# Kernel optimization log

Measured on AMD Instinct MI355X. Metric: run time of the kernel, lower is better.

The kernel has to match this reference:

```python
import jax, jax.numpy as jnp
import numpy as np

N = 100000          # num_nodes
E = 1600000         # num_edges
D_IN = 128          # in_channels
H = 128             # hidden_channels
D_OUT = 128         # out_channels


def setup_inputs() -> dict:
    key = jax.random.key(0)
    ks = jax.random.split(key, 12)
    s = 1.0 / np.sqrt(H)
    inp = {
        "x": jax.random.normal(ks[0], (N, D_IN), dtype=jnp.float32),
        "edge_index": jax.random.randint(ks[1], (2, E), 0, N, dtype=jnp.int64),
        "edge_weight": jax.random.uniform(ks[2], (E,), dtype=jnp.float32),
        # edge_lin (SparseLinear): weight [num_nodes, hidden], bias [hidden]
        "W_edge": jax.random.uniform(ks[3], (N, H), jnp.float32, -1.0 / np.sqrt(N), 1.0 / np.sqrt(N)),
        "b_edge": jax.random.uniform(ks[4], (H,), jnp.float32, -1.0 / np.sqrt(N), 1.0 / np.sqrt(N)),
        # node_mlp: single Linear(in_channels, hidden)
        "W_node": jax.random.uniform(ks[5], (D_IN, H), jnp.float32, -1.0 / np.sqrt(D_IN), 1.0 / np.sqrt(D_IN)),
        "b_node": jax.random.uniform(ks[6], (H,), jnp.float32, -1.0 / np.sqrt(D_IN), 1.0 / np.sqrt(D_IN)),
        # cat_lin1 / cat_lin2: Linear(hidden, hidden)
        "W_cat1": jax.random.uniform(ks[7], (H, H), jnp.float32, -s, s),
        "b_cat1": jax.random.uniform(ks[8], (H,), jnp.float32, -s, s),
        "W_cat2": jax.random.uniform(ks[9], (H, H), jnp.float32, -s, s),
        "b_cat2": jax.random.uniform(ks[10], (H,), jnp.float32, -s, s),
        # final_mlp: single Linear(hidden, out_channels)
        "W_final": jax.random.uniform(ks[11], (H, D_OUT), jnp.float32, -s, s),
        "b_final": jax.random.uniform(jax.random.fold_in(key, 99), (D_OUT,), jnp.float32, -s, s),
    }
    return inp


def reference(x, edge_index, edge_weight, W_edge, b_edge, W_node, b_node,
              W_cat1, b_cat1, W_cat2, b_cat2, W_final, b_final):
    num_nodes = W_edge.shape[0]
    src, dst = edge_index[0], edge_index[1]
    # SparseLinear: out[i] = sum_{(j,i)} edge_weight * W_edge[j]  (SpMM A @ W)
    msg = edge_weight[:, None] * W_edge[src]                      # [E, H]
    out = jax.ops.segment_sum(msg, dst, num_segments=num_nodes)  # [N, H]
    out = out + b_edge
    # out = out + cat_lin1(out)
    out = out + out @ W_cat1 + b_cat1
    # x branch: node_mlp (single linear), then residual adds
    xh = x @ W_node + b_node                                      # [N, H]
    out = out + xh
    out = out + xh @ W_cat2 + b_cat2
    # final_mlp(relu(out)): single linear
    return jax.nn.relu(out) @ W_final + b_final
```

## Files before the change

### kernel.cpp

```cpp
#include <hip/hip_runtime.h>
#include <hip/hip_fp16.h>

#define NN 100000
#define NE 1600000
#define H  128
#define CAP 48

typedef short short8 __attribute__((ext_vector_type(8)));
typedef float f32x4 __attribute__((ext_vector_type(4)));

__device__ __forceinline__ unsigned short f2bf(float f) {
    unsigned int u = __float_as_uint(f);
    u = (u + 0x7fffu + ((u >> 16) & 1u)) >> 16;
    return (unsigned short)u;
}
__device__ __forceinline__ unsigned int packbf(float a, float b) {
    return (unsigned int)f2bf(a) | ((unsigned int)f2bf(b) << 16);
}
__device__ __forceinline__ unsigned char f2e5m2(float f) {
    unsigned short h = __half_as_ushort(__float2half_rn(f));
    h = (unsigned short)(h + 0x7F + ((h >> 8) & 1));
    return (unsigned char)(h >> 8);
}
__device__ __forceinline__ float e5m2lo(unsigned int u) {
    return __half2float(__ushort_as_half((unsigned short)((u << 8) & 0xFF00)));
}
__device__ __forceinline__ float e5m2hi(unsigned int u) {
    return __half2float(__ushort_as_half((unsigned short)(u & 0xFF00)));
}
__device__ __forceinline__ float entw(unsigned int e) {
    return __half2float(__ushort_as_half((unsigned short)((e & 0x7FFFu) << 1)));
}

__global__ void fill_kernel(const int* __restrict__ ei, const float* __restrict__ ew,
                            int* __restrict__ deg, unsigned int* __restrict__ bkt) {
    int e = blockIdx.x * 256 + threadIdx.x;
    if (e >= NE) return;
    int d = ei[NE + e];
    int pos = atomicAdd(&deg[d], 1);
    if (pos < CAP) {
        unsigned short h = __half_as_ushort(__float2half_rn(ew[e]));
        bkt[d * CAP + pos] = ((unsigned int)ei[e] << 15) | (h >> 1);
    }
}

__global__ __launch_bounds__(128) void prep_weights(const float* __restrict__ W_node,
                                                    const float* __restrict__ W_cat1,
                                                    const float* __restrict__ W_cat2,
                                                    const float* __restrict__ W_final,
                                                    const float* __restrict__ b_edge,
                                                    const float* __restrict__ b_node,
                                                    const float* __restrict__ b_cat1,
                                                    const float* __restrict__ b_cat2,
                                                    unsigned short* __restrict__ m2_t,
                                                    unsigned short* __restrict__ w3_t,
                                                    unsigned short* __restrict__ wf_t,
                                                    float* __restrict__ b4,
                                                    int* __restrict__ deg) {
    int t = threadIdx.x;
    int n = blockIdx.x;
    if (n < H) {
        __shared__ float c2col[H];
        c2col[t] = W_cat2[t * H + n];
        __syncthreads();
        float dot = 0.f;
        #pragma unroll 8
        for (int j = 0; j < H; ++j)
            dot += W_node[t * H + j] * c2col[j];
        float w3 = W_node[t * H + n] + dot;
        m2_t[n * H + t] = f2bf(W_cat1[t * H + n] + (t == n ? 1.f : 0.f));
        w3_t[n * H + t] = f2bf(w3);
        wf_t[n * H + t] = f2bf(W_final[t * H + n]);
    } else if (n == H) {
        __shared__ float be[H], bn[H];
        be[t] = b_edge[t];
        bn[t] = b_node[t];
        __syncthreads();
        float acc = be[t] + bn[t] + b_cat1[t] + b_cat2[t];
        for (int j = 0; j < H; ++j)
            acc += be[j] * W_cat1[j * H + t] + bn[j] * W_cat2[j * H + t];
        b4[t] = acc;
    } else {
        int i = (n - H - 1) * 128 + t;
        if (i < NN) deg[i] = 0;
    }
}

__global__ __launch_bounds__(256) void gemm_we2(const float* __restrict__ W_edge,
                                                const unsigned short* __restrict__ m2_t,
                                                unsigned char* __restrict__ we8,
                                                int nrows) {
    const int TR = 32;
    __shared__ unsigned int Wsb[TR][64];
    int row0 = blockIdx.x * TR;
    int tid = threadIdx.x;

    for (int i = tid; i < TR * H / 4; i += 256) {
        int fi = i * 4;
        int rr = fi >> 7, cc = fi & 127;
        float4 v = {0.f, 0.f, 0.f, 0.f};
        if (row0 + rr < nrows)
            v = *reinterpret_cast<const float4*>(&W_edge[(long long)(row0 + rr) * H + cc]);
        int sw = (rr & 7) << 2;
        Wsb[rr][(cc >> 1) ^ sw]       = packbf(v.x, v.y);
        Wsb[rr][((cc >> 1) + 1) ^ sw] = packbf(v.z, v.w);
    }
    __syncthreads();

    int wv = tid >> 6, lane = tid & 63;
    int rt = wv & 1, ctb = (tid >> 7) * 4;
    int l15 = lane & 15, lhi = lane >> 4;
    int arow = rt * 16 + l15, asw = arow & 7;

    f32x4 zero4 = {0.f, 0.f, 0.f, 0.f};
    f32x4 acc[4];
    acc[0] = zero4; acc[1] = zero4; acc[2] = zero4; acc[3] = zero4;
    const short8* wrow = reinterpret_cast<const short8*>(&Wsb[arow][0]);

    #pragma unroll
    for (int kt = 0; kt < 4; ++kt) {
        short8 afrag = wrow[(kt * 4 + lhi) ^ asw];
        #pragma unroll
        for (int j = 0; j < 4; ++j) {
            short8 bfrag = *reinterpret_cast<const short8*>(
                &m2_t[((ctb + j) * 16 + l15) * H + kt * 32 + lhi * 8]);
            acc[j] = __builtin_amdgcn_mfma_f32_16x16x32_bf16(afrag, bfrag, acc[j], 0, 0, 0);
        }
    }

    #pragma unroll
    for (int j = 0; j < 4; ++j) {
        int colg = (ctb + j) * 16 + l15;
        #pragma unroll
        for (int r = 0; r < 4; ++r) {
            int row = row0 + rt * 16 + lhi * 4 + r;
            if (row < nrows)
                we8[(long long)row * H + colg] = f2e5m2(acc[j][r]);
        }
    }
}

#define EDGE2(jv, ax, ay)                                                   \
    {                                                                       \
        unsigned int e0 = bkt[jv];                                          \
        unsigned int e1 = bkt[jv + 1];                                      \
        unsigned int u0 = we8u[(e0 >> 15) * 64 + lane];                     \
        unsigned int u1 = we8u[(e1 >> 15) * 64 + lane];                     \
        float w0 = entw(e0), w1 = entw(e1);                                 \
        ax += w0 * e5m2lo(u0) + w1 * e5m2lo(u1);                            \
        ay += w0 * e5m2hi(u0) + w1 * e5m2hi(u1);                            \
    }

#define EDGE1(jv, ax, ay)                                                   \
    {                                                                       \
        unsigned int e = bkt[jv];                                           \
        unsigned int u = we8u[(e >> 15) * 64 + lane];                       \
        float w = entw(e);                                                  \
        ax += w * e5m2lo(u);                                                \
        ay += w * e5m2hi(u);                                                \
    }

#define STEP8(eN0, eN1, uN0, uN1, jv, ax, ay)                               \
    {                                                                       \
        float w0 = entw(eN0), w1 = entw(eN1);                               \
        ax += w0 * e5m2lo(uN0) + w1 * e5m2lo(uN1);                          \
        ay += w0 * e5m2hi(uN0) + w1 * e5m2hi(uN1);                          \
        jv += 2;                                                            \
    }

__global__ __launch_bounds__(256) void gather_fused(const int* __restrict__ deg,
                                                    const unsigned int* __restrict__ bkt,
                                                    const unsigned short* __restrict__ we8u,
                                                    const float* __restrict__ x,
                                                    const unsigned short* __restrict__ w3_t,
                                                    const float* __restrict__ b4,
                                                    const unsigned short* __restrict__ wf_t,
                                                    const float* __restrict__ bf,
                                                    float* __restrict__ out,
                                                    int nrows) {
    const int TR = 32;
    __shared__ unsigned int Xsb[TR][64];
    __shared__ float Gs[TR][132];
    int row0 = blockIdx.x * TR;
    int tid = threadIdx.x;

    for (int i = tid; i < TR * H / 4; i += 256) {
        int fi = i * 4;
        int rr = fi >> 7, cc = fi & 127;
        float4 xv = *reinterpret_cast<const float4*>(&x[(long long)(row0 + rr) * H + cc]);
        int sw = (rr & 7) << 2;
        Xsb[rr][(cc >> 1) ^ sw]       = packbf(xv.x, xv.y);
        Xsb[rr][((cc >> 1) + 1) ^ sw] = packbf(xv.z, xv.w);
    }

    int wv = tid >> 6;
    int lane = tid & 63;
    {
        int base = row0 + wv * 8;
        float axA = 0.f, ayA = 0.f, axB = 0.f, ayB = 0.f;
        float axC = 0.f, ayC = 0.f, axD = 0.f, ayD = 0.f;
        float axE = 0.f, ayE = 0.f, axF = 0.f, ayF = 0.f;
        float axG = 0.f, ayG = 0.f, axH = 0.f, ayH = 0.f;

        int dgA = __builtin_amdgcn_readfirstlane(deg[base]);
        int dgB = __builtin_amdgcn_readfirstlane(deg[base + 1]);
        int dgC = __builtin_amdgcn_readfirstlane(deg[base + 2]);
        int dgD = __builtin_amdgcn_readfirstlane(deg[base + 3]);
        int dgE = __builtin_amdgcn_readfirstlane(deg[base + 4]);
        int dgF = __builtin_amdgcn_readfirstlane(deg[base + 5]);
        int dgG = __builtin_amdgcn_readfirstlane(deg[base + 6]);
        int dgH = __builtin_amdgcn_readfirstlane(deg[base + 7]);
        if (dgA > CAP) dgA = CAP;
        if (dgB > CAP) dgB = CAP;
        if (dgC > CAP) dgC = CAP;
        if (dgD > CAP) dgD = CAP;
        if (dgE > CAP) dgE = CAP;
        if (dgF > CAP) dgF = CAP;
        if (dgG > CAP) dgG = CAP;
        if (dgH > CAP) dgH = CAP;
        int jA = base * CAP,        i1A = jA + dgA;
        int jB = (base + 1) * CAP,  i1B = jB + dgB;
        int jC = (base + 2) * CAP,  i1C = jC + dgC;
        int jD = (base + 3) * CAP,  i1D = jD + dgD;
        int jE = (base + 4) * CAP,  i1E = jE + dgE;
        int jF = (base + 5) * CAP,  i1F = jF + dgF;
        int jG = (base + 6) * CAP,  i1G = jG + dgG;
        int jH = (base + 7) * CAP,  i1H = jH + dgH;

        while (jA + 2 <= i1A && jB + 2 <= i1B && jC + 2 <= i1C && jD + 2 <= i1D &&
               jE + 2 <= i1E && jF + 2 <= i1F && jG + 2 <= i1G && jH + 2 <= i1H) {
            unsigned int eA0 = bkt[jA], eA1 = bkt[jA + 1];
            unsigned int eB0 = bkt[jB], eB1 = bkt[jB + 1];
            unsigned int eC0 = bkt[jC], eC1 = bkt[jC + 1];
            unsigned int eD0 = bkt[jD], eD1 = bkt[jD + 1];
            unsigned int eE0 = bkt[jE], eE1 = bkt[jE + 1];
            unsigned int eF0 = bkt[jF], eF1 = bkt[jF + 1];
            unsigned int eG0 = bkt[jG], eG1 = bkt[jG + 1];
            unsigned int eH0 = bkt[jH], eH1 = bkt[jH + 1];
            unsigned int uA0 = we8u[(eA0 >> 15) * 64 + lane];
            unsigned int uA1 = we8u[(eA1 >> 15) * 64 + lane];
            unsigned int uB0 = we8u[(eB0 >> 15) * 64 + lane];
            unsigned int uB1 = we8u[(eB1 >> 15) * 64 + lane];
            unsigned int uC0 = we8u[(eC0 >> 15) * 64 + lane];
            unsigned int uC1 = we8u[(eC1 >> 15) * 64 + lane];
            unsigned int uD0 = we8u[(eD0 >> 15) * 64 + lane];
            unsigned int uD1 = we8u[(eD1 >> 15) * 64 + lane];
            unsigned int uE0 = we8u[(eE0 >> 15) * 64 + lane];
            unsigned int uE1 = we8u[(eE1 >> 15) * 64 + lane];
            unsigned int uF0 = we8u[(eF0 >> 15) * 64 + lane];
            unsigned int uF1 = we8u[(eF1 >> 15) * 64 + lane];
            unsigned int uG0 = we8u[(eG0 >> 15) * 64 + lane];
            unsigned int uG1 = we8u[(eG1 >> 15) * 64 + lane];
            unsigned int uH0 = we8u[(eH0 >> 15) * 64 + lane];
            unsigned int uH1 = we8u[(eH1 >> 15) * 64 + lane];
            STEP8(eA0, eA1, uA0, uA1, jA, axA, ayA)
            STEP8(eB0, eB1, uB0, uB1, jB, axB, ayB)
            STEP8(eC0, eC1, uC0, uC1, jC, axC, ayC)
            STEP8(eD0, eD1, uD0, uD1, jD, axD, ayD)
            STEP8(eE0, eE1, uE0, uE1, jE, axE, ayE)
            STEP8(eF0, eF1, uF0, uF1, jF, axF, ayF)
            STEP8(eG0, eG1, uG0, uG1, jG, axG, ayG)
            STEP8(eH0, eH1, uH0, uH1, jH, axH, ayH)
        }
        while (jA + 2 <= i1A && jB + 2 <= i1B) { EDGE2(jA, axA, ayA) EDGE2(jB, axB, ayB) jA += 2; jB += 2; }
        for (; jA + 2 <= i1A; jA += 2) EDGE2(jA, axA, ayA)
        if (jA < i1A) EDGE1(jA, axA, ayA)
        for (; jB + 2 <= i1B; jB += 2) EDGE2(jB, axB, ayB)
        if (jB < i1B) EDGE1(jB, axB, ayB)
        while (jC + 2 <= i1C && jD + 2 <= i1D) { EDGE2(jC, axC, ayC) EDGE2(jD, axD, ayD) jC += 2; jD += 2; }
        for (; jC + 2 <= i1C; jC += 2) EDGE2(jC, axC, ayC)
        if (jC < i1C) EDGE1(jC, axC, ayC)
        for (; jD + 2 <= i1D; jD += 2) EDGE2(jD, axD, ayD)
        if (jD < i1D) EDGE1(jD, axD, ayD)
        while (jE + 2 <= i1E && jF + 2 <= i1F) { EDGE2(jE, axE, ayE) EDGE2(jF, axF, ayF) jE += 2; jF += 2; }
        for (; jE + 2 <= i1E; jE += 2) EDGE2(jE, axE, ayE)
        if (jE < i1E) EDGE1(jE, axE, ayE)
        for (; jF + 2 <= i1F; jF += 2) EDGE2(jF, axF, ayF)
        if (jF < i1F) EDGE1(jF, axF, ayF)
        while (jG + 2 <= i1G && jH + 2 <= i1H) { EDGE2(jG, axG, ayG) EDGE2(jH, axH, ayH) jG += 2; jH += 2; }
        for (; jG + 2 <= i1G; jG += 2) EDGE2(jG, axG, ayG)
        if (jG < i1G) EDGE1(jG, axG, ayG)
        for (; jH + 2 <= i1H; jH += 2) EDGE2(jH, axH, ayH)
        if (jH < i1H) EDGE1(jH, axH, ayH)

        int rr = wv * 8;
        *reinterpret_cast<float2*>(&Gs[rr][2 * lane])     = make_float2(axA, ayA);
        *reinterpret_cast<float2*>(&Gs[rr + 1][2 * lane]) = make_float2(axB, ayB);
        *reinterpret_cast<float2*>(&Gs[rr + 2][2 * lane]) = make_float2(axC, ayC);
        *reinterpret_cast<float2*>(&Gs[rr + 3][2 * lane]) = make_float2(axD, ayD);
        *reinterpret_cast<float2*>(&Gs[rr + 4][2 * lane]) = make_float2(axE, ayE);
        *reinterpret_cast<float2*>(&Gs[rr + 5][2 * lane]) = make_float2(axF, ayF);
        *reinterpret_cast<float2*>(&Gs[rr + 6][2 * lane]) = make_float2(axG, ayG);
        *reinterpret_cast<float2*>(&Gs[rr + 7][2 * lane]) = make_float2(axH, ayH);
    }
    __syncthreads();

    int rt = wv & 1, ctb = (tid >> 7) * 4;
    int l15 = lane & 15, lhi = lane >> 4;
    int arow = rt * 16 + l15, asw = arow & 7;

    f32x4 acc[4];
    #pragma unroll
    for (int j = 0; j < 4; ++j) {
        int colg = (ctb + j) * 16 + l15;
        float bv = b4[colg];
        #pragma unroll
        for (int r = 0; r < 4; ++r)
            acc[j][r] = Gs[rt * 16 + lhi * 4 + r][colg] + bv;
    }
    __syncthreads();

    const short8* xsrow = reinterpret_cast<const short8*>(&Xsb[arow][0]);
    #pragma unroll
    for (int kt = 0; kt < 4; ++kt) {
        short8 afrag = xsrow[(kt * 4 + lhi) ^ asw];
        #pragma unroll
        for (int j = 0; j < 4; ++j) {
            short8 bfrag = *reinterpret_cast<const short8*>(
                &w3_t[((ctb + j) * 16 + l15) * H + kt * 32 + lhi * 8]);
            acc[j] = __builtin_amdgcn_mfma_f32_16x16x32_bf16(afrag, bfrag, acc[j], 0, 0, 0);
        }
    }

    unsigned short* t4s = reinterpret_cast<unsigned short*>(Gs);
    #pragma unroll
    for (int j = 0; j < 4; ++j) {
        int colg = (ctb + j) * 16 + l15;
        #pragma unroll
        for (int r = 0; r < 4; ++r) {
            int row = rt * 16 + lhi * 4 + r;
            float v = fmaxf(acc[j][r], 0.f);
            t4s[row * 128 + (colg ^ ((row & 7) << 3))] = f2bf(v);
        }
    }
    __syncthreads();

    f32x4 zero4 = {0.f, 0.f, 0.f, 0.f};
    f32x4 acc2[4];
    acc2[0] = zero4; acc2[1] = zero4; acc2[2] = zero4; acc2[3] = zero4;
    const short8* t4row = reinterpret_cast<const short8*>(t4s + arow * 128);

    #pragma unroll
    for (int kt = 0; kt < 4; ++kt) {
        short8 afrag = t4row[(kt * 4 + lhi) ^ asw];
        #pragma unroll
        for (int j = 0; j < 4; ++j) {
            short8 bfrag = *reinterpret_cast<const short8*>(
                &wf_t[((ctb + j) * 16 + l15) * H + kt * 32 + lhi * 8]);
            acc2[j] = __builtin_amdgcn_mfma_f32_16x16x32_bf16(afrag, bfrag, acc2[j], 0, 0, 0);
        }
    }

    #pragma unroll
    for (int j = 0; j < 4; ++j) {
        int colg = (ctb + j) * 16 + l15;
        float bv = bf[colg];
        #pragma unroll
        for (int r = 0; r < 4; ++r) {
            int row = row0 + rt * 16 + lhi * 4 + r;
            out[(long long)row * H + colg] = acc2[j][r] + bv;
        }
    }
}

extern "C" void kernel_launch(void* const* d_in, const int* in_sizes, int n_in,
                              void* d_out, int out_size, void* d_ws, size_t ws_size,
                              hipStream_t stream) {
    const float* x       = (const float*)d_in[0];
    const int*   ei      = (const int*)d_in[1];
    const float* ew      = (const float*)d_in[2];
    const float* W_edge  = (const float*)d_in[3];
    const float* b_edge  = (const float*)d_in[4];
    const float* W_node  = (const float*)d_in[5];
    const float* b_node  = (const float*)d_in[6];
    const float* W_cat1  = (const float*)d_in[7];
    const float* b_cat1  = (const float*)d_in[8];
    const float* W_cat2  = (const float*)d_in[9];
    const float* b_cat2  = (const float*)d_in[10];
    const float* W_final = (const float*)d_in[11];
    const float* b_final = (const float*)d_in[12];
    float* out = (float*)d_out;

    int* deg = (int*)d_ws;
    unsigned int* bkt = (unsigned int*)(deg + NN);
    unsigned char* we8 = (unsigned char*)(bkt + (size_t)NN * CAP);
    unsigned short* m2_t = (unsigned short*)(we8 + (size_t)NN * H);
    unsigned short* w3_t = m2_t + H * H;
    unsigned short* wf_t = w3_t + H * H;
    float* b4 = (float*)(wf_t + H * H);

    int zero_blocks = (NN + 127) / 128;
    prep_weights<<<H + 1 + zero_blocks, H, 0, stream>>>(W_node, W_cat1, W_cat2, W_final,
                                                        b_edge, b_node, b_cat1, b_cat2,
                                                        m2_t, w3_t, wf_t, b4, deg);
    fill_kernel<<<(NE + 255) / 256, 256, 0, stream>>>(ei, ew, deg, bkt);

    gemm_we2<<<(NN + 31) / 32, 256, 0, stream>>>(W_edge, m2_t, we8, NN);

    gather_fused<<<(NN + 31) / 32, 256, 0, stream>>>(deg, bkt, (const unsigned short*)we8,
                                                     x, w3_t, b4, wf_t, b_final, out, NN);
}
```

Baseline: 297.2 us.

## Move cat_lin1 GEMM after aggregation and merge W_edge conversion into prep kernel

Instead of precomputing W_edge·(I+W_cat1) over all 100k rows before the gather, W_edge is simply quantised to e5m2 in a combined prep kernel. The aggregated rows are packed to bf16 in shared memory and multiplied by m2 via MFMA inside the fused gather kernel, alongside the x·w3 product. This removes the separate GEMM kernel launch and its dependency on prepared weights. The cost is extra MFMA work and B-fragment loads per block in the gather kernel, plus bf16 rounding of the aggregated sums.

```diff
diff --git a/kernel.cpp b/kernel.cpp
--- a/kernel.cpp
+++ b/kernel.cpp
@@ -5,6 +5,9 @@
 #define NE 1600000
 #define H  128
 #define CAP 48
+#define CONV_BLKS 6250
+#define PREP_BLKS 64
+#define ZERO_BLKS ((NN + 255) / 256)
 
 typedef short short8 __attribute__((ext_vector_type(8)));
 typedef float f32x4 __attribute__((ext_vector_type(4)));
@@ -30,6 +33,71 @@
 }
 __device__ __forceinline__ float entw(unsigned int e) {
     return __half2float(__ushort_as_half((unsigned short)((e & 0x7FFFu) << 1)));
+}
+
+__global__ __launch_bounds__(256) void conv_prep(const float* __restrict__ W_edge,
+                                                 const float* __restrict__ W_node,
+                                                 const float* __restrict__ W_cat1,
+                                                 const float* __restrict__ W_cat2,
+                                                 const float* __restrict__ W_final,
+                                                 const float* __restrict__ b_edge,
+                                                 const float* __restrict__ b_node,
+                                                 const float* __restrict__ b_cat1,
+                                                 const float* __restrict__ b_cat2,
+                                                 unsigned char* __restrict__ we8,
+                                                 unsigned short* __restrict__ m2_t,
+                                                 unsigned short* __restrict__ w3_t,
+                                                 unsigned short* __restrict__ wf_t,
+                                                 float* __restrict__ b4,
+                                                 int* __restrict__ deg) {
+    int b = blockIdx.x;
+    int t = threadIdx.x;
+    if (b < CONV_BLKS) {
+        long long i = (long long)b * 2048 + t * 8;
+        float4 v0 = *reinterpret_cast<const float4*>(&W_edge[i]);
+        float4 v1 = *reinterpret_cast<const float4*>(&W_edge[i + 4]);
+        unsigned long long o = 0;
+        o |= (unsigned long long)f2e5m2(v0.x);
+        o |= (unsigned long long)f2e5m2(v0.y) << 8;
+        o |= (unsigned long long)f2e5m2(v0.z) << 16;
+        o |= (unsigned long long)f2e5m2(v0.w) << 24;
+        o |= (unsigned long long)f2e5m2(v1.x) << 32;
+        o |= (unsigned long long)f2e5m2(v1.y) << 40;
+        o |= (unsigned long long)f2e5m2(v1.z) << 48;
+        o |= (unsigned long long)f2e5m2(v1.w) << 56;
+        *reinterpret_cast<unsigned long long*>(&we8[i]) = o;
+    } else if (b < CONV_BLKS + PREP_BLKS) {
+        int p = b - CONV_BLKS;
+        int half = t >> 7, tt = t & 127;
+        int n = p * 2 + half;
+        __shared__ float c2col[2][H];
+        c2col[half][tt] = W_cat2[tt * H + n];
+        __syncthreads();
+        float dot = 0.f;
+        #pragma unroll 8
+        for (int j = 0; j < H; ++j)
+            dot += W_node[tt * H + j] * c2col[half][j];
+        float w3 = W_node[tt * H + n] + dot;
+        m2_t[n * H + tt] = f2bf(W_cat1[tt * H + n] + (tt == n ? 1.f : 0.f));
+        w3_t[n * H + tt] = f2bf(w3);
+        wf_t[n * H + tt] = f2bf(W_final[tt * H + n]);
+    } else if (b == CONV_BLKS + PREP_BLKS) {
+        __shared__ float be[H], bn[H];
+        if (t < H) {
+            be[t] = b_edge[t];
+            bn[t] = b_node[t];
+        }
+        __syncthreads();
+        if (t < H) {
+            float acc = be[t] + bn[t] + b_cat1[t] + b_cat2[t];
+            for (int j = 0; j < H; ++j)
+                acc += be[j] * W_cat1[j * H + t] + bn[j] * W_cat2[j * H + t];
+            b4[t] = acc;
+        }
+    } else {
+        int i = (b - CONV_BLKS - PREP_BLKS - 1) * 256 + t;
+        if (i < NN) deg[i] = 0;
+    }
 }
 
 __global__ void fill_kernel(const int* __restrict__ ei, const float* __restrict__ ew,
@@ -44,102 +112,6 @@
     }
 }
 
-__global__ __launch_bounds__(128) void prep_weights(const float* __restrict__ W_node,
-                                                    const float* __restrict__ W_cat1,
-                                                    const float* __restrict__ W_cat2,
-                                                    const float* __restrict__ W_final,
-                                                    const float* __restrict__ b_edge,
-                                                    const float* __restrict__ b_node,
-                                                    const float* __restrict__ b_cat1,
-                                                    const float* __restrict__ b_cat2,
-                                                    unsigned short* __restrict__ m2_t,
-                                                    unsigned short* __restrict__ w3_t,
-                                                    unsigned short* __restrict__ wf_t,
-                                                    float* __restrict__ b4,
-                                                    int* __restrict__ deg) {
-    int t = threadIdx.x;
-    int n = blockIdx.x;
-    if (n < H) {
-        __shared__ float c2col[H];
-        c2col[t] = W_cat2[t * H + n];
-        __syncthreads();
-        float dot = 0.f;
-        #pragma unroll 8
-        for (int j = 0; j < H; ++j)
-            dot += W_node[t * H + j] * c2col[j];
-        float w3 = W_node[t * H + n] + dot;
-        m2_t[n * H + t] = f2bf(W_cat1[t * H + n] + (t == n ? 1.f : 0.f));
-        w3_t[n * H + t] = f2bf(w3);
-        wf_t[n * H + t] = f2bf(W_final[t * H + n]);
-    } else if (n == H) {
-        __shared__ float be[H], bn[H];
-        be[t] = b_edge[t];
-        bn[t] = b_node[t];
-        __syncthreads();
-        float acc = be[t] + bn[t] + b_cat1[t] + b_cat2[t];
-        for (int j = 0; j < H; ++j)
-            acc += be[j] * W_cat1[j * H + t] + bn[j] * W_cat2[j * H + t];
-        b4[t] = acc;
-    } else {
-        int i = (n - H - 1) * 128 + t;
-        if (i < NN) deg[i] = 0;
-    }
-}
-
-__global__ __launch_bounds__(256) void gemm_we2(const float* __restrict__ W_edge,
-                                                const unsigned short* __restrict__ m2_t,
-                                                unsigned char* __restrict__ we8,
-                                                int nrows) {
-    const int TR = 32;
-    __shared__ unsigned int Wsb[TR][64];
-    int row0 = blockIdx.x * TR;
-    int tid = threadIdx.x;
-
-    for (int i = tid; i < TR * H / 4; i += 256) {
-        int fi = i * 4;
-        int rr = fi >> 7, cc = fi & 127;
-        float4 v = {0.f, 0.f, 0.f, 0.f};
-        if (row0 + rr < nrows)
-            v = *reinterpret_cast<const float4*>(&W_edge[(long long)(row0 + rr) * H + cc]);
-        int sw = (rr & 7) << 2;
-        Wsb[rr][(cc >> 1) ^ sw]       = packbf(v.x, v.y);
-        Wsb[rr][((cc >> 1) + 1) ^ sw] = packbf(v.z, v.w);
-    }
-    __syncthreads();
-
-    int wv = tid >> 6, lane = tid & 63;
-    int rt = wv & 1, ctb = (tid >> 7) * 4;
-    int l15 = lane & 15, lhi = lane >> 4;
-    int arow = rt * 16 + l15, asw = arow & 7;
-
-    f32x4 zero4 = {0.f, 0.f, 0.f, 0.f};
-    f32x4 acc[4];
-    acc[0] = zero4; acc[1] = zero4; acc[2] = zero4; acc[3] = zero4;
-    const short8* wrow = reinterpret_cast<const short8*>(&Wsb[arow][0]);
-
-    #pragma unroll
-    for (int kt = 0; kt < 4; ++kt) {
-        short8 afrag = wrow[(kt * 4 + lhi) ^ asw];
-        #pragma unroll
-        for (int j = 0; j < 4; ++j) {
-            short8 bfrag = *reinterpret_cast<const short8*>(
-                &m2_t[((ctb + j) * 16 + l15) * H + kt * 32 + lhi * 8]);
-            acc[j] = __builtin_amdgcn_mfma_f32_16x16x32_bf16(afrag, bfrag, acc[j], 0, 0, 0);
-        }
-    }
-
-    #pragma unroll
-    for (int j = 0; j < 4; ++j) {
-        int colg = (ctb + j) * 16 + l15;
-        #pragma unroll
-        for (int r = 0; r < 4; ++r) {
-            int row = row0 + rt * 16 + lhi * 4 + r;
-            if (row < nrows)
-                we8[(long long)row * H + colg] = f2e5m2(acc[j][r]);
-        }
-    }
-}
-
 #define EDGE2(jv, ax, ay)                                                   \
     {                                                                       \
         unsigned int e0 = bkt[jv];                                          \
@@ -172,6 +144,7 @@
                                                     const unsigned int* __restrict__ bkt,
                                                     const unsigned short* __restrict__ we8u,
                                                     const float* __restrict__ x,
+                                                    const unsigned short* __restrict__ m2_t,
                                                     const unsigned short* __restrict__ w3_t,
                                                     const float* __restrict__ b4,
                                                     const unsigned short* __restrict__ wf_t,
@@ -180,7 +153,7 @@
                                                     int nrows) {
     const int TR = 32;
     __shared__ unsigned int Xsb[TR][64];
-    __shared__ float Gs[TR][132];
+    __shared__ unsigned int Gsb[TR][64];
     int row0 = blockIdx.x * TR;
     int tid = threadIdx.x;
 
@@ -284,14 +257,14 @@
         if (jH < i1H) EDGE1(jH, axH, ayH)
 
         int rr = wv * 8;
-        *reinterpret_cast<float2*>(&Gs[rr][2 * lane])     = make_float2(axA, ayA);
-        *reinterpret_cast<float2*>(&Gs[rr + 1][2 * lane]) = make_float2(axB, ayB);
-        *reinterpret_cast<float2*>(&Gs[rr + 2][2 * lane]) = make_float2(axC, ayC);
-        *reinterpret_cast<float2*>(&Gs[rr + 3][2 * lane]) = make_float2(axD, ayD);
-        *reinterpret_cast<float2*>(&Gs[rr + 4][2 * lane]) = make_float2(axE, ayE);
-        *reinterpret_cast<float2*>(&Gs[rr + 5][2 * lane]) = make_float2(axF, ayF);
-        *reinterpret_cast<float2*>(&Gs[rr + 6][2 * lane]) = make_float2(axG, ayG);
-        *reinterpret_cast<float2*>(&Gs[rr + 7][2 * lane]) = make_float2(axH, ayH);
+        Gsb[rr][lane ^ ((rr & 7) << 2)]             = packbf(axA, ayA);
+        Gsb[rr + 1][lane ^ (((rr + 1) & 7) << 2)]   = packbf(axB, ayB);
+        Gsb[rr + 2][lane ^ (((rr + 2) & 7) << 2)]   = packbf(axC, ayC);
+        Gsb[rr + 3][lane ^ (((rr + 3) & 7) << 2)]   = packbf(axD, ayD);
+        Gsb[rr + 4][lane ^ (((rr + 4) & 7) << 2)]   = packbf(axE, ayE);
+        Gsb[rr + 5][lane ^ (((rr + 5) & 7) << 2)]   = packbf(axF, ayF);
+        Gsb[rr + 6][lane ^ (((rr + 6) & 7) << 2)]   = packbf(axG, ayG);
+        Gsb[rr + 7][lane ^ (((rr + 7) & 7) << 2)]   = packbf(axH, ayH);
     }
     __syncthreads();
 
@@ -302,27 +275,29 @@
     f32x4 acc[4];
     #pragma unroll
     for (int j = 0; j < 4; ++j) {
-        int colg = (ctb + j) * 16 + l15;
-        float bv = b4[colg];
-        #pragma unroll
-        for (int r = 0; r < 4; ++r)
-            acc[j][r] = Gs[rt * 16 + lhi * 4 + r][colg] + bv;
-    }
-    __syncthreads();
-
+        float bv = b4[(ctb + j) * 16 + l15];
+        acc[j][0] = bv; acc[j][1] = bv; acc[j][2] = bv; acc[j][3] = bv;
+    }
+
+    const short8* gsrow = reinterpret_cast<const short8*>(&Gsb[arow][0]);
     const short8* xsrow = reinterpret_cast<const short8*>(&Xsb[arow][0]);
     #pragma unroll
     for (int kt = 0; kt < 4; ++kt) {
-        short8 afrag = xsrow[(kt * 4 + lhi) ^ asw];
+        short8 afragG = gsrow[(kt * 4 + lhi) ^ asw];
+        short8 afragX = xsrow[(kt * 4 + lhi) ^ asw];
         #pragma unroll
         for (int j = 0; j < 4; ++j) {
-            short8 bfrag = *reinterpret_cast<const short8*>(
+            short8 bm2 = *reinterpret_cast<const short8*>(
+                &m2_t[((ctb + j) * 16 + l15) * H + kt * 32 + lhi * 8]);
+            short8 bw3 = *reinterpret_cast<const short8*>(
                 &w3_t[((ctb + j) * 16 + l15) * H + kt * 32 + lhi * 8]);
-            acc[j] = __builtin_amdgcn_mfma_f32_16x16x32_bf16(afrag, bfrag, acc[j], 0, 0, 0);
-        }
-    }
-
-    unsigned short* t4s = reinterpret_cast<unsigned short*>(Gs);
+            acc[j] = __builtin_amdgcn_mfma_f32_16x16x32_bf16(afragG, bm2, acc[j], 0, 0, 0);
+            acc[j] = __builtin_amdgcn_mfma_f32_16x16x32_bf16(afragX, bw3, acc[j], 0, 0, 0);
+        }
+    }
+    __syncthreads();
+
+    unsigned short* t4s = reinterpret_cast<unsigned short*>(Gsb);
     #pragma unroll
     for (int j = 0; j < 4; ++j) {
         int colg = (ctb + j) * 16 + l15;
@@ -389,14 +364,13 @@
     unsigned short* wf_t = w3_t + H * H;
     float* b4 = (float*)(wf_t + H * H);
 
-    int zero_blocks = (NN + 127) / 128;
-    prep_weights<<<H + 1 + zero_blocks, H, 0, stream>>>(W_node, W_cat1, W_cat2, W_final,
-                                                        b_edge, b_node, b_cat1, b_cat2,
-                                                        m2_t, w3_t, wf_t, b4, deg);
+    conv_prep<<<CONV_BLKS + PREP_BLKS + 1 + ZERO_BLKS, 256, 0, stream>>>(
+        W_edge, W_node, W_cat1, W_cat2, W_final,
+        b_edge, b_node, b_cat1, b_cat2,
+        we8, m2_t, w3_t, wf_t, b4, deg);
+
     fill_kernel<<<(NE + 255) / 256, 256, 0, stream>>>(ei, ew, deg, bkt);
 
-    gemm_we2<<<(NN + 31) / 32, 256, 0, stream>>>(W_edge, m2_t, we8, NN);
-
     gather_fused<<<(NN + 31) / 32, 256, 0, stream>>>(deg, bkt, (const unsigned short*)we8,
-                                                     x, w3_t, b4, wf_t, b_final, out, NN);
-}
+                                                     x, m2_t, w3_t, b4, wf_t, b_final, out, NN);
+}
```

New measurement: 280.1 us, median of 2. -5.7%, faster.
